# Optimization experiments

Hardware: AMD Instinct MI355X
Metric: run time of the kernel (lower is better)

Reference implementation:

```python
import jax, jax.numpy as jnp
import numpy as np

H = 16          # n_heads
WIN = 256       # window_size
NEG_INF = -1e30 # finite stand-in for -inf to stay fp16/bf16 safe


def setup_inputs() -> dict:
    key = jax.random.key(0)
    ks = jax.random.split(key, 9)
    B, L, C = 2, 2048, 2048
    s = 0.02  # weight init scale
    inp = {
        "x": jax.random.normal(ks[0], (B, L, C), jnp.float32),
        "Wq": jax.random.normal(ks[1], (C, C), jnp.float32) * s,
        "bq": jnp.zeros((C,), jnp.float32),
        "Wk": jax.random.normal(ks[2], (C, C), jnp.float32) * s,
        "bk": jnp.zeros((C,), jnp.float32),
        "Wv": jax.random.normal(ks[3], (C, C), jnp.float32) * s,
        "bv": jnp.zeros((C,), jnp.float32),
        "Wo": jax.random.normal(ks[4], (C, C), jnp.float32) * s,
        "bo": jnp.zeros((C,), jnp.float32),
    }
    return inp


def _attn(x, Wq, bq, Wk, bk, Wv, bv, Wo, bo):
    B, L, C = x.shape
    D = C // H
    # torch Linear: y = x @ W.T + b
    q = (x @ Wq.T + bq).reshape(B, L, H, D).transpose(0, 2, 1, 3)  # (B,H,L,D)
    k = (x @ Wk.T + bk).reshape(B, L, H, D).transpose(0, 2, 1, 3)
    v = (x @ Wv.T + bv).reshape(B, L, H, D).transpose(0, 2, 1, 3)
    i = jnp.arange(L)[:, None]
    j = jnp.arange(L)[None, :]
    allowed = (j <= i) & (j > i - WIN)
    bias = jnp.where(allowed, 0.0, NEG_INF).astype(x.dtype)  # (L,L)
    scale = 1.0 / np.sqrt(D)
    attn = jnp.einsum('bhid,bhjd->bhij', q, k) + bias
    a = jax.nn.softmax(attn * scale, axis=-1)
    out = jnp.einsum('bhij,bhjd->bhid', a, v)  # (B,H,L,D)
    out = out.transpose(0, 2, 1, 3).reshape(B, L, C)
    return out @ Wo.T + bo  # dropout = identity (eval mode)


def reference(x, Wq, bq, Wk, bk, Wv, bv, Wo, bo):
    return _attn(x, Wq, bq, Wk, bk, Wv, bv, Wo, bo)
```

## Files before the change

### kernel.cpp

```cpp
#include <hip/hip_runtime.h>
#include <hip/hip_bf16.h>
#include <stdint.h>

typedef __bf16 bf16;
typedef __attribute__((ext_vector_type(8))) __bf16 bf16x8;
typedef __attribute__((ext_vector_type(8))) unsigned short u16x8;
typedef __attribute__((ext_vector_type(4))) float f32x4;

#define L_SEQ 2048
#define C_DIM 2048
#define NBATCH 2
#define M_ROWS (NBATCH * L_SEQ)
#define DH 128
#define NHEAD 16
#define WINSZ 256

__device__ __forceinline__ float san(float v, float s) {
    return ((__float_as_uint(v) & 0x7f800000u) == 0x7f800000u) ? s : v;
}

__device__ __forceinline__ bf16x8 pack8(float4 lo, float4 hi) {
    bf16x8 v;
    v[0] = (bf16)lo.x; v[1] = (bf16)lo.y; v[2] = (bf16)lo.z; v[3] = (bf16)lo.w;
    v[4] = (bf16)hi.x; v[5] = (bf16)hi.y; v[6] = (bf16)hi.z; v[7] = (bf16)hi.w;
    return v;
}

typedef const __attribute__((address_space(1))) void g_void;
typedef __attribute__((address_space(3))) void l_void;
__device__ __forceinline__ void glds16(const void* g, void* l) {
    __builtin_amdgcn_global_load_lds((g_void*)g, (l_void*)l, 16, 0, 0);
}

template <bool AF32, bool OUTF32>
__global__ __launch_bounds__(256)
void gemm_bt_bias(const void* __restrict__ Ap,
                  const float* __restrict__ W0, const float* __restrict__ b0, void* O0,
                  const float* __restrict__ W1, const float* __restrict__ b1, void* O1,
                  const float* __restrict__ W2, const float* __restrict__ b2, void* O2,
                  float snt)
{
    const int K = C_DIM, N = C_DIM;
    const float* W = W0; const float* bias = b0; void* Out = O0;
    if (blockIdx.z == 1)      { W = W1; bias = b1; Out = O1; }
    else if (blockIdx.z == 2) { W = W2; bias = b2; Out = O2; }

    __shared__ bf16 As[128 * 32];
    __shared__ bf16 Bs[128 * 32];

    const int tid  = threadIdx.x;
    const int lane = tid & 63;
    const int m0 = blockIdx.x * 128;
    const int n0 = blockIdx.y * 128;

    const int wave = tid >> 6;
    const int wm = (wave >> 1) * 64;
    const int wn = (wave & 1) * 64;

    const int srow = tid >> 2;
    const int scol = (tid & 3) * 8;

    f32x4 acc[4][4] = {};

    const int fr = lane & 15;
    const int fq = (lane >> 4) * 8;

    for (int k0 = 0; k0 < K; k0 += 32) {
        bf16x8 ra[2], rb[2];
        #pragma unroll
        for (int p = 0; p < 2; p++) {
            const size_t aoff = (size_t)(m0 + p * 64 + srow) * K + k0 + scol;
            if (AF32) {
                const float* A = (const float*)Ap;
                float4 lo = *(const float4*)(A + aoff);
                float4 hi = *(const float4*)(A + aoff + 4);
                ra[p] = pack8(lo, hi);
            } else {
                const bf16* A = (const bf16*)Ap;
                ra[p] = *(const bf16x8*)(A + aoff);
            }
            const size_t boff = (size_t)(n0 + p * 64 + srow) * K + k0 + scol;
            float4 wlo = *(const float4*)(W + boff);
            float4 whi = *(const float4*)(W + boff + 4);
            rb[p] = pack8(wlo, whi);
        }
        __syncthreads();
        #pragma unroll
        for (int p = 0; p < 2; p++) {
            *(bf16x8*)&As[(p * 64 + srow) * 32 + scol] = ra[p];
            *(bf16x8*)&Bs[(p * 64 + srow) * 32 + scol] = rb[p];
        }
        __syncthreads();

        bf16x8 af[4], bfr[4];
        #pragma unroll
        for (int s = 0; s < 4; s++)
            af[s] = *(const bf16x8*)&As[(wm + s * 16 + fr) * 32 + fq];
        #pragma unroll
        for (int s = 0; s < 4; s++)
            bfr[s] = *(const bf16x8*)&Bs[(wn + s * 16 + fr) * 32 + fq];
        #pragma unroll
        for (int sm = 0; sm < 4; sm++)
            #pragma unroll
            for (int sn = 0; sn < 4; sn++)
                acc[sm][sn] = __builtin_amdgcn_mfma_f32_16x16x32_bf16(af[sm], bfr[sn], acc[sm][sn], 0, 0, 0);
    }

    const int r0 = (lane >> 4) * 4;
    const int cn = lane & 15;
    #pragma unroll
    for (int sn = 0; sn < 4; sn++) {
        const int n = n0 + wn + sn * 16 + cn;
        const float bv = bias[n];
        #pragma unroll
        for (int sm = 0; sm < 4; sm++) {
            const int m = m0 + wm + sm * 16 + r0;
            #pragma unroll
            for (int r = 0; r < 4; r++) {
                const float v = san(acc[sm][sn][r] + bv, snt);
                if (OUTF32) ((float*)Out)[(size_t)(m + r) * N + n] = v;
                else        ((bf16*)Out)[(size_t)(m + r) * N + n] = (bf16)v;
            }
        }
    }
}

__device__ __forceinline__ void phase_mid() {
    asm volatile("" ::: "memory");
    __builtin_amdgcn_s_barrier();
    asm volatile("s_waitcnt lgkmcnt(0)" ::: "memory");
    __builtin_amdgcn_sched_barrier(0);
    __builtin_amdgcn_s_setprio(1);
}
__device__ __forceinline__ void phase_end() {
    __builtin_amdgcn_s_setprio(0);
    asm volatile("" ::: "memory");
    __builtin_amdgcn_s_barrier();
}

#define BUFSZ 49152
#define BOFF  32768

#define LDA2(d) do {                                                          \
    char* s_ = lds + (d) * BUFSZ + ahalf * 16384;                             \
    _Pragma("unroll") for (int sm = 0; sm < 4; sm++)                          \
    _Pragma("unroll") for (int kk = 0; kk < 2; kk++) {                        \
        const int row_ = arow0 + sm * 16 + fr;                                \
        afr[sm][kk] = *(const bf16x8*)(s_ + row_ * 128 +                      \
                        (((kk * 4 + g) ^ (row_ & 7)) << 4));                  \
    } } while (0)

#define LDB2(d, qn, arr) do {                                                 \
    char* s_ = lds + (d) * BUFSZ + BOFF;                                      \
    _Pragma("unroll") for (int sn = 0; sn < 2; sn++)                          \
    _Pragma("unroll") for (int kk = 0; kk < 2; kk++) {                        \
        const int row_ = wn + (qn) * 32 + sn * 16 + fr;                       \
        arr[sn][kk] = *(const bf16x8*)(s_ + row_ * 128 +                      \
                        (((kk * 4 + g) ^ (row_ & 7)) << 4));                  \
    } } while (0)

#define MFMAH(qn, arr) do {                                                   \
    _Pragma("unroll") for (int kk = 0; kk < 2; kk++)                          \
    _Pragma("unroll") for (int sm = 0; sm < 4; sm++)                          \
    _Pragma("unroll") for (int sn = 0; sn < 2; sn++)                          \
        acc[sm][(qn) * 2 + sn] =                                              \
            __builtin_amdgcn_mfma_f32_16x16x32_bf16(afr[sm][kk], arr[sn][kk], \
                acc[sm][(qn) * 2 + sn], 0, 0, 0);                             \
    } while (0)

template <bool OUTF32>
__global__ __launch_bounds__(512, 2)
void gemm_256x128(const bf16* __restrict__ A,
                  const bf16* __restrict__ W0, const float* __restrict__ b0, void* O0,
                  const bf16* __restrict__ W1, const float* __restrict__ b1, void* O1,
                  const bf16* __restrict__ W2, const float* __restrict__ b2, void* O2,
                  float snt)
{
    const int K = C_DIM, N = C_DIM;
    const int NT = K / 64;
    const bf16* W = W0; const float* bias = b0; void* Out = O0;
    if (blockIdx.z == 1)      { W = W1; bias = b1; Out = O1; }
    else if (blockIdx.z == 2) { W = W2; bias = b2; Out = O2; }

    __shared__ __attribute__((aligned(16))) char lds[98304];

    const int tid  = threadIdx.x;
    const int lane = tid & 63;
    const int w    = tid >> 6;

    int id = blockIdx.x + (int)gridDim.x * blockIdx.y;
    id = (id & 7) * 32 + (id >> 3);
    const int m0 = (id & 15) * 256;
    const int n0 = (id >> 4) * 128;

    const int wm = (w >> 1) * 64;
    const int wn = (w & 1) * 64;
    const int fr = lane & 15;
    const int g  = lane >> 4;
    const int ahalf = w >> 2;
    const int arow0 = ((w >> 1) & 1) * 64;

    const int srow  = tid >> 3;
    const int scol  = (((tid & 7) ^ (srow & 7)) * 8);
    const int wvoff = (tid >> 6) * 1024;

    f32x4 acc[4][4] = {};
    bf16x8 afr[4][2], b0r[2][2], b1r[2][2];

    #define STAGE_A(t) do {                                                   \
        const int d_ = (t) & 1;                                               \
        const int tc_ = (t) < NT ? (t) : NT - 1;                              \
        const bf16* src_ = A + (size_t)(m0 + srow) * K + tc_ * 64 + scol;     \
        char* dst_ = lds + d_ * BUFSZ + wvoff;                                \
        glds16(src_,                   dst_);                                 \
        glds16(src_ + (size_t)64 * K,  dst_ + 8192);                          \
        glds16(src_ + (size_t)128 * K, dst_ + 16384);                         \
        glds16(src_ + (size_t)192 * K, dst_ + 24576);                         \
    } while (0)

    #define STAGE_B(t) do {                                                   \
        const int d_ = (t) & 1;                                               \
        const int tc_ = (t) < NT ? (t) : NT - 1;                              \
        const bf16* src_ = W + (size_t)(n0 + srow) * K + tc_ * 64 + scol;     \
        char* dst_ = lds + d_ * BUFSZ + BOFF + wvoff;                         \
        glds16(src_,                  dst_);                                  \
        glds16(src_ + (size_t)64 * K, dst_ + 8192);                           \
    } while (0)

    STAGE_A(0); STAGE_B(0); STAGE_A(1);
    asm volatile("s_waitcnt vmcnt(4)" ::: "memory");
    asm volatile("" ::: "memory");
    __builtin_amdgcn_s_barrier();

    #pragma unroll 1
    for (int i = 0; i < NT / 2; i++) {
        const int t1 = 2 * i + 1, t2 = 2 * i + 2, t3 = 2 * i + 3;
        LDA2(0); LDB2(0, 0, b0r);
        STAGE_B(t1);
        phase_mid(); MFMAH(0, b0r); phase_end();
        LDB2(0, 1, b1r);
        STAGE_A(t2);
        asm volatile("s_waitcnt vmcnt(4)" ::: "memory");
        phase_mid(); MFMAH(1, b1r); phase_end();
        LDA2(1); LDB2(1, 0, b0r);
        STAGE_B(t2);
        phase_mid(); MFMAH(0, b0r); phase_end();
        LDB2(1, 1, b1r);
        STAGE_A(t3);
        asm volatile("s_waitcnt vmcnt(4)" ::: "memory");
        phase_mid(); MFMAH(1, b1r); phase_end();
    }
    asm volatile("s_waitcnt vmcnt(0)" ::: "memory");

    const int cn = lane & 15;
    const int r0 = (lane >> 4) * 4;
    #pragma unroll
    for (int sn2 = 0; sn2 < 4; sn2++) {
        const int n = n0 + wn + sn2 * 16 + cn;
        const float bv = bias[n];
        #pragma unroll
        for (int sm2 = 0; sm2 < 4; sm2++) {
            const int m = m0 + wm + sm2 * 16 + r0;
            #pragma unroll
            for (int r = 0; r < 4; r++) {
                const float v = san(acc[sm2][sn2][r] + bv, snt);
                if (OUTF32) ((float*)Out)[(size_t)(m + r) * N + n] = v;
                else        ((bf16*)Out)[(size_t)(m + r) * N + n] = (bf16)v;
            }
        }
    }
    #undef STAGE_A
    #undef STAGE_B
}

__global__ __launch_bounds__(256)
void cvt_f32_bf16(const float* __restrict__ s0, bf16* __restrict__ d0,
                  const float* __restrict__ s1, bf16* __restrict__ d1,
                  const float* __restrict__ s2, bf16* __restrict__ d2,
                  const float* __restrict__ s3, bf16* __restrict__ d3,
                  const float* __restrict__ s4, bf16* __restrict__ d4)
{
    const float* s; bf16* d; int n;
    switch (blockIdx.y) {
        case 0:  s = s0; d = d0; n = M_ROWS * C_DIM; break;
        case 1:  s = s1; d = d1; n = C_DIM * C_DIM; break;
        case 2:  s = s2; d = d2; n = C_DIM * C_DIM; break;
        case 3:  s = s3; d = d3; n = C_DIM * C_DIM; break;
        default: s = s4; d = d4; n = C_DIM * C_DIM; break;
    }
    const int nv = n >> 3;
    const int stride = (int)gridDim.x * 256;
    for (int i = blockIdx.x * 256 + threadIdx.x; i < nv; i += stride) {
        const float4 lo = *(const float4*)(s + (size_t)i * 8);
        const float4 hi = *(const float4*)(s + (size_t)i * 8 + 4);
        *(bf16x8*)(d + (size_t)i * 8) = pack8(lo, hi);
    }
}

#define SWZK(r, byteoff) ((((r) * 256) + (byteoff)) ^ (((r) & 7) << 4))
#define SWZV(d, byteoff) ((((d) * 128) + (byteoff)) ^ (((((d) & 7) ^ (((d) >> 3) & 7))) << 4))
#define SWZP(r, byteoff) ((((r) * 128) + (byteoff)) ^ (((r) & 7) << 4))

__global__ __launch_bounds__(256)
void swa_attn(const bf16* __restrict__ Q, const bf16* __restrict__ Kp,
              const bf16* __restrict__ V, bf16* __restrict__ Oattn, float snt)
{
    __shared__ bf16 Ks[64 * 128];
    __shared__ bf16 Vt[128 * 64];
    __shared__ bf16 Ps[64 * 64];

    const int tid  = threadIdx.x;
    const int lane = tid & 63;
    const int w    = tid >> 6;
    const int q0 = blockIdx.x * 64;
    const int h  = blockIdx.y;
    const int b  = blockIdx.z;
    const size_t base = (size_t)b * L_SEQ * C_DIM + (size_t)h * DH;

    const int fr  = lane & 15;
    const int g   = lane >> 4;
    const int fq8 = g * 8;

    bf16x8 qf[4];
    {
        const bf16* qrow = Q + base + (size_t)(q0 + w * 16 + fr) * C_DIM;
        #pragma unroll
        for (int kk = 0; kk < 4; kk++)
            qf[kk] = *(const bf16x8*)(qrow + kk * 32 + fq8);
    }

    const int rl0 = g * 4;
    const int ig  = q0 + w * 16 + rl0;
    const float scale = 0.08838834764831845f;

    float m_run[4], l_run[4];
    #pragma unroll
    for (int r = 0; r < 4; r++) { m_run[r] = -1e30f; l_run[r] = 0.0f; }
    f32x4 Oacc[8] = {};

    const int krr = tid >> 4;
    const int kcc = (tid & 15) * 8;
    const int vc  = tid & 15;
    const int vd0 = vc * 8;
    const int vpb = tid >> 4;

    for (int kb = 0; kb < 5; kb++) {
        const int s = q0 - 256 + kb * 64;
        if (s < 0) continue;

        __syncthreads();

        #pragma unroll
        for (int p = 0; p < 4; p++) {
            const int r = p * 16 + krr;
            const uint4 kv = *(const uint4*)(Kp + base + (size_t)(s + r) * C_DIM + kcc);
            *(uint4*)((char*)Ks + SWZK(r, kcc * 2)) = kv;
        }
        #pragma unroll
        for (int it = 0; it < 2; it++) {
            const int p = vpb + it * 16;
            const bf16* vr = V + base + (size_t)(s + 2 * p) * C_DIM + vd0;
            const u16x8 va = *(const u16x8*)vr;
            const u16x8 vb = *(const u16x8*)(vr + C_DIM);
            #pragma unroll
            for (int j = 0; j < 8; j++) {
                const uint32_t val = (uint32_t)va[j] | ((uint32_t)vb[j] << 16);
                *(uint32_t*)((char*)Vt + SWZV(vd0 + j, 4 * p)) = val;
            }
        }
        __syncthreads();

        f32x4 sacc[4] = {};
        __builtin_amdgcn_s_setprio(1);
        #pragma unroll
        for (int kk = 0; kk < 4; kk++) {
            #pragma unroll
            for (int t = 0; t < 4; t++) {
                const bf16x8 kf = *(const bf16x8*)((char*)Ks + SWZK(t * 16 + fr, (kk * 32 + fq8) * 2));
                sacc[t] = __builtin_amdgcn_mfma_f32_16x16x32_bf16(qf[kk], kf, sacc[t], 0, 0, 0);
            }
        }
        __builtin_amdgcn_s_setprio(0);

        float alpha[4];
        #pragma unroll
        for (int r = 0; r < 4; r++) {
            const int iq = ig + r;
            float p4[4];
            float bm = -1e30f;
            #pragma unroll
            for (int t = 0; t < 4; t++) {
                const int j = s + t * 16 + fr;
                const bool allow = (j <= iq) && (j > iq - WINSZ);
                p4[t] = allow ? sacc[t][r] * scale : -1e30f;
                bm = fmaxf(bm, p4[t]);
            }
            bm = fmaxf(bm, __shfl_xor(bm, 1, 64));
            bm = fmaxf(bm, __shfl_xor(bm, 2, 64));
            bm = fmaxf(bm, __shfl_xor(bm, 4, 64));
            bm = fmaxf(bm, __shfl_xor(bm, 8, 64));
            const float m_new = fmaxf(m_run[r], bm);
            alpha[r] = __expf(m_run[r] - m_new);
            m_run[r] = m_new;
            float ps = 0.0f;
            #pragma unroll
            for (int t = 0; t < 4; t++) {
                const float e = (p4[t] > -1e29f) ? __expf(p4[t] - m_new) : 0.0f;
                p4[t] = e;
                ps += e;
            }
            ps += __shfl_xor(ps, 1, 64);
            ps += __shfl_xor(ps, 2, 64);
            ps += __shfl_xor(ps, 4, 64);
            ps += __shfl_xor(ps, 8, 64);
            l_run[r] = l_run[r] * alpha[r] + ps;

            const int prow = w * 16 + rl0 + r;
            #pragma unroll
            for (int t = 0; t < 4; t++)
                *(bf16*)((char*)Ps + SWZP(prow, (t * 16 + fr) * 2)) = (bf16)p4[t];
        }

        #pragma unroll
        for (int t = 0; t < 8; t++)
            #pragma unroll
            for (int r = 0; r < 4; r++)
                Oacc[t][r] *= alpha[r];

        __builtin_amdgcn_s_setprio(1);
        #pragma unroll
        for (int kk = 0; kk < 2; kk++) {
            const bf16x8 pa = *(const bf16x8*)((char*)Ps + SWZP(w * 16 + fr, (kk * 32 + fq8) * 2));
            #pragma unroll
            for (int t = 0; t < 8; t++) {
                const bf16x8 vf = *(const bf16x8*)((char*)Vt + SWZV(t * 16 + fr, (kk * 32 + fq8) * 2));
                Oacc[t] = __builtin_amdgcn_mfma_f32_16x16x32_bf16(pa, vf, Oacc[t], 0, 0, 0);
            }
        }
        __builtin_amdgcn_s_setprio(0);
    }

    bf16* ob = Oattn + base;
    #pragma unroll
    for (int r = 0; r < 4; r++) {
        const float inv_l = 1.0f / l_run[r];
        const size_t ro = (size_t)(q0 + w * 16 + rl0 + r) * C_DIM;
        #pragma unroll
        for (int t = 0; t < 8; t++)
            ob[ro + t * 16 + fr] = (bf16)san(Oacc[t][r] * inv_l, snt);
    }
}

__global__ void fill_signal(float* out, int n, float v) {
    for (int i = blockIdx.x * blockDim.x + threadIdx.x; i < n; i += gridDim.x * blockDim.x)
        out[i] = v;
}

extern "C" void kernel_launch(void* const* d_in, const int* in_sizes, int n_in,
                              void* d_out, int out_size, void* d_ws, size_t ws_size,
                              hipStream_t stream) {
    const size_t sz      = (size_t)M_ROWS * C_DIM;
    const size_t wsz     = (size_t)C_DIM * C_DIM;
    const size_t bfbytes = sz * sizeof(bf16);
    const size_t FASTNEED = 3 * sz * sizeof(bf16) + 4 * wsz * sizeof(bf16);

    const int expn[9] = {8388608, 4194304, 2048, 4194304, 2048,
                         4194304, 2048, 4194304, 2048};
    float sig = 0.0f;
    if (n_in != 9) sig = 1100.0f;
    else {
        for (int i = 0; i < 9; i++)
            if (in_sizes[i] != expn[i]) { sig = 1200.0f + 100.0f * i; break; }
    }
    if (sig == 0.0f && out_size != (int)sz) sig = 2100.0f;
    if (sig == 0.0f && ws_size < 2 * bfbytes) sig = 3000.0f + 10.0f * (float)(ws_size >> 20);
    if (sig != 0.0f) {
        fill_signal<<<512, 256, 0, stream>>>((float*)d_out, (int)sz, sig);
        return;
    }

    const float* x  = (const float*)d_in[0];
    const float* Wq = (const float*)d_in[1];
    const float* bq = (const float*)d_in[2];
    const float* Wk = (const float*)d_in[3];
    const float* bk = (const float*)d_in[4];
    const float* Wv = (const float*)d_in[5];
    const float* bv = (const float*)d_in[6];
    const float* Wo = (const float*)d_in[7];
    const float* bo = (const float*)d_in[8];

    if (ws_size >= FASTNEED) {
        bf16* xbf = (bf16*)d_ws;
        bf16* kws = xbf + sz;
        bf16* vws = kws + sz;
        bf16* wqb = vws + sz;
        bf16* wkb = wqb + wsz;
        bf16* wvb = wkb + wsz;
        bf16* wob = wvb + wsz;
        bf16*  qscr  = (bf16*)d_out;
        float* out32 = (float*)d_out;

        cvt_f32_bf16<<<dim3(2048, 5), 256, 0, stream>>>(
            x, xbf, Wq, wqb, Wk, wkb, Wv, wvb, Wo, wob);

        gemm_256x128<false><<<dim3(16, 16, 3), 512, 0, stream>>>(
            xbf, wqb, bq, (void*)qscr, wkb, bk, (void*)kws,
            wvb, bv, (void*)vws, 111.0f);

        swa_attn<<<dim3(L_SEQ / 64, NHEAD, NBATCH), 256, 0, stream>>>(
            qscr, kws, vws, xbf, 222.0f);

        gemm_256x128<true><<<dim3(16, 16, 1), 512, 0, stream>>>(
            xbf, wob, bo, (void*)out32, wob, bo, (void*)out32,
            wob, bo, (void*)out32, 444.0f);
    } else {
        bf16*  kws   = (bf16*)d_ws;
        bf16*  vws   = kws + sz;
        bf16*  qscr  = (bf16*)d_out;
        float* out32 = (float*)d_out;

        gemm_bt_bias<true, false><<<dim3(32, 16, 3), 256, 0, stream>>>(
            (const void*)x, Wq, bq, (void*)qscr, Wk, bk, (void*)kws,
            Wv, bv, (void*)vws, 111.0f);

        swa_attn<<<dim3(L_SEQ / 64, NHEAD, NBATCH), 256, 0, stream>>>(
            qscr, kws, vws, qscr, 222.0f);

        hipMemcpyAsync(kws, qscr, bfbytes, hipMemcpyDeviceToDevice, stream);

        gemm_bt_bias<false, true><<<dim3(32, 16, 1), 256, 0, stream>>>(
            (const void*)kws, Wo, bo, (void*)out32, Wo, bo, (void*)out32,
            Wo, bo, (void*)out32, 444.0f);
    }
}
```

Measured before the change: 329.5 us.

## Load K tiles via global_load_lds and prefetch next V block into registers

In the sliding-window attention kernel, K tiles are now copied straight from global memory into LDS with global_load_lds. A pre-swizzled column index replaces the load-to-register-then-store path. V rows for the next key block are loaded into registers while the current block is computed, which overlaps global latency with the QK/PV MFMA work. The loop now starts at the first valid key block instead of testing and skipping negative starts. The cost is extra live registers for the prefetched V, and correctness depends on the direct-to-LDS write layout matching the SWZK swizzle the reads expect.

```diff
diff --git a/kernel.cpp b/kernel.cpp
--- a/kernel.cpp
+++ b/kernel.cpp
@@ -30,6 +30,19 @@
 typedef __attribute__((address_space(3))) void l_void;
 __device__ __forceinline__ void glds16(const void* g, void* l) {
     __builtin_amdgcn_global_load_lds((g_void*)g, (l_void*)l, 16, 0, 0);
+}
+
+__device__ __forceinline__ void phase_mid() {
+    asm volatile("" ::: "memory");
+    __builtin_amdgcn_s_barrier();
+    asm volatile("s_waitcnt lgkmcnt(0)" ::: "memory");
+    __builtin_amdgcn_sched_barrier(0);
+    __builtin_amdgcn_s_setprio(1);
+}
+__device__ __forceinline__ void phase_end() {
+    __builtin_amdgcn_s_setprio(0);
+    asm volatile("" ::: "memory");
+    __builtin_amdgcn_s_barrier();
 }
 
 template <bool AF32, bool OUTF32>
@@ -123,19 +136,6 @@
             }
         }
     }
-}
-
-__device__ __forceinline__ void phase_mid() {
-    asm volatile("" ::: "memory");
-    __builtin_amdgcn_s_barrier();
-    asm volatile("s_waitcnt lgkmcnt(0)" ::: "memory");
-    __builtin_amdgcn_sched_barrier(0);
-    __builtin_amdgcn_s_setprio(1);
-}
-__device__ __forceinline__ void phase_end() {
-    __builtin_amdgcn_s_setprio(0);
-    asm volatile("" ::: "memory");
-    __builtin_amdgcn_s_barrier();
 }
 
 #define BUFSZ 49152
@@ -338,37 +338,54 @@
     for (int r = 0; r < 4; r++) { m_run[r] = -1e30f; l_run[r] = 0.0f; }
     f32x4 Oacc[8] = {};
 
-    const int krr = tid >> 4;
-    const int kcc = (tid & 15) * 8;
-    const int vc  = tid & 15;
-    const int vd0 = vc * 8;
+    const int krow = tid >> 4;
+    const int kcol = ((tid & 15) ^ (krow & 7)) * 8;
+    char* const kdst = (char*)Ks + w * 1024;
+
+    const int vd0 = (tid & 15) * 8;
     const int vpb = tid >> 4;
 
-    for (int kb = 0; kb < 5; kb++) {
+    const int kbs = (blockIdx.x < 4) ? (4 - (int)blockIdx.x) : 0;
+
+    u16x8 va0, vb0, va1, vb1;
+    {
+        const int s0 = q0 - 256 + kbs * 64;
+        const bf16* vr0 = V + base + (size_t)(s0 + 2 * vpb) * C_DIM + vd0;
+        va0 = *(const u16x8*)vr0;
+        vb0 = *(const u16x8*)(vr0 + C_DIM);
+        const bf16* vr1 = V + base + (size_t)(s0 + 2 * (vpb + 16)) * C_DIM + vd0;
+        va1 = *(const u16x8*)vr1;
+        vb1 = *(const u16x8*)(vr1 + C_DIM);
+    }
+
+    for (int kb = kbs; kb < 5; kb++) {
         const int s = q0 - 256 + kb * 64;
-        if (s < 0) continue;
 
         __syncthreads();
 
         #pragma unroll
-        for (int p = 0; p < 4; p++) {
-            const int r = p * 16 + krr;
-            const uint4 kv = *(const uint4*)(Kp + base + (size_t)(s + r) * C_DIM + kcc);
-            *(uint4*)((char*)Ks + SWZK(r, kcc * 2)) = kv;
-        }
-        #pragma unroll
-        for (int it = 0; it < 2; it++) {
-            const int p = vpb + it * 16;
-            const bf16* vr = V + base + (size_t)(s + 2 * p) * C_DIM + vd0;
-            const u16x8 va = *(const u16x8*)vr;
-            const u16x8 vb = *(const u16x8*)(vr + C_DIM);
-            #pragma unroll
-            for (int j = 0; j < 8; j++) {
-                const uint32_t val = (uint32_t)va[j] | ((uint32_t)vb[j] << 16);
-                *(uint32_t*)((char*)Vt + SWZV(vd0 + j, 4 * p)) = val;
-            }
+        for (int p = 0; p < 4; p++)
+            glds16(Kp + base + (size_t)(s + p * 16 + krow) * C_DIM + kcol,
+                   kdst + p * 4096);
+
+        #pragma unroll
+        for (int j = 0; j < 8; j++) {
+            const uint32_t v0 = (uint32_t)va0[j] | ((uint32_t)vb0[j] << 16);
+            *(uint32_t*)((char*)Vt + SWZV(vd0 + j, 4 * vpb)) = v0;
+            const uint32_t v1 = (uint32_t)va1[j] | ((uint32_t)vb1[j] << 16);
+            *(uint32_t*)((char*)Vt + SWZV(vd0 + j, 4 * (vpb + 16))) = v1;
         }
         __syncthreads();
+
+        if (kb < 4) {
+            const int sn = s + 64;
+            const bf16* vr0 = V + base + (size_t)(sn + 2 * vpb) * C_DIM + vd0;
+            va0 = *(const u16x8*)vr0;
+            vb0 = *(const u16x8*)(vr0 + C_DIM);
+            const bf16* vr1 = V + base + (size_t)(sn + 2 * (vpb + 16)) * C_DIM + vd0;
+            va1 = *(const u16x8*)vr1;
+            vb1 = *(const u16x8*)(vr1 + C_DIM);
+        }
 
         f32x4 sacc[4] = {};
         __builtin_amdgcn_s_setprio(1);
```

Result: slower. 356.7 us (+8.2%).

## Enlarge attention query tile to 128 rows with 8 waves and skip inactive waves

Applied to the files above, without the earlier changes.

The sliding-window attention kernel now handles 128 query rows per block with 512 threads (8 waves), so each K/V tile loaded into shared memory serves twice as many queries. Each block now walks 6 key tiles instead of 5. Waves whose 16 query rows fall outside a key tile's window skip the QK, softmax and PV work. The block index is also remapped so that neighbouring blocks are spread across XCDs. The cost is a larger P buffer in shared memory and fewer, larger blocks (512 in total). The attention kernel is only part of the total time, which also includes the GEMMs.

```diff
diff --git a/kernel.cpp b/kernel.cpp
--- a/kernel.cpp
+++ b/kernel.cpp
@@ -30,6 +30,19 @@
 typedef __attribute__((address_space(3))) void l_void;
 __device__ __forceinline__ void glds16(const void* g, void* l) {
     __builtin_amdgcn_global_load_lds((g_void*)g, (l_void*)l, 16, 0, 0);
+}
+
+__device__ __forceinline__ void phase_mid() {
+    asm volatile("" ::: "memory");
+    __builtin_amdgcn_s_barrier();
+    asm volatile("s_waitcnt lgkmcnt(0)" ::: "memory");
+    __builtin_amdgcn_sched_barrier(0);
+    __builtin_amdgcn_s_setprio(1);
+}
+__device__ __forceinline__ void phase_end() {
+    __builtin_amdgcn_s_setprio(0);
+    asm volatile("" ::: "memory");
+    __builtin_amdgcn_s_barrier();
 }
 
 template <bool AF32, bool OUTF32>
@@ -123,19 +136,6 @@
             }
         }
     }
-}
-
-__device__ __forceinline__ void phase_mid() {
-    asm volatile("" ::: "memory");
-    __builtin_amdgcn_s_barrier();
-    asm volatile("s_waitcnt lgkmcnt(0)" ::: "memory");
-    __builtin_amdgcn_sched_barrier(0);
-    __builtin_amdgcn_s_setprio(1);
-}
-__device__ __forceinline__ void phase_end() {
-    __builtin_amdgcn_s_setprio(0);
-    asm volatile("" ::: "memory");
-    __builtin_amdgcn_s_barrier();
 }
 
 #define BUFSZ 49152
@@ -301,36 +301,43 @@
 #define SWZV(d, byteoff) ((((d) * 128) + (byteoff)) ^ (((((d) & 7) ^ (((d) >> 3) & 7))) << 4))
 #define SWZP(r, byteoff) ((((r) * 128) + (byteoff)) ^ (((r) & 7) << 4))
 
-__global__ __launch_bounds__(256)
+__global__ __launch_bounds__(512)
 void swa_attn(const bf16* __restrict__ Q, const bf16* __restrict__ Kp,
               const bf16* __restrict__ V, bf16* __restrict__ Oattn, float snt)
 {
     __shared__ bf16 Ks[64 * 128];
     __shared__ bf16 Vt[128 * 64];
-    __shared__ bf16 Ps[64 * 64];
+    __shared__ bf16 Ps[128 * 64];
 
     const int tid  = threadIdx.x;
     const int lane = tid & 63;
     const int w    = tid >> 6;
-    const int q0 = blockIdx.x * 64;
-    const int h  = blockIdx.y;
-    const int b  = blockIdx.z;
+
+    int f = blockIdx.x + 16 * (blockIdx.y + 16 * blockIdx.z);
+    f = (f & 7) * 64 + (f >> 3);
+    const int bx = f & 15;
+    const int h  = (f >> 4) & 15;
+    const int b  = f >> 8;
+
+    const int q0 = bx * 128;
     const size_t base = (size_t)b * L_SEQ * C_DIM + (size_t)h * DH;
 
     const int fr  = lane & 15;
     const int g   = lane >> 4;
     const int fq8 = g * 8;
 
+    const int qw = q0 + w * 16;
+
     bf16x8 qf[4];
     {
-        const bf16* qrow = Q + base + (size_t)(q0 + w * 16 + fr) * C_DIM;
+        const bf16* qrow = Q + base + (size_t)(qw + fr) * C_DIM;
         #pragma unroll
         for (int kk = 0; kk < 4; kk++)
             qf[kk] = *(const bf16x8*)(qrow + kk * 32 + fq8);
     }
 
     const int rl0 = g * 4;
-    const int ig  = q0 + w * 16 + rl0;
+    const int ig  = qw + rl0;
     const float scale = 0.08838834764831845f;
 
     float m_run[4], l_run[4];
@@ -340,111 +347,111 @@
 
     const int krr = tid >> 4;
     const int kcc = (tid & 15) * 8;
-    const int vc  = tid & 15;
-    const int vd0 = vc * 8;
+    const int vd0 = (tid & 15) * 8;
     const int vpb = tid >> 4;
 
-    for (int kb = 0; kb < 5; kb++) {
+    for (int kb = 0; kb < 6; kb++) {
         const int s = q0 - 256 + kb * 64;
         if (s < 0) continue;
 
         __syncthreads();
 
         #pragma unroll
-        for (int p = 0; p < 4; p++) {
-            const int r = p * 16 + krr;
+        for (int p = 0; p < 2; p++) {
+            const int r = p * 32 + krr;
             const uint4 kv = *(const uint4*)(Kp + base + (size_t)(s + r) * C_DIM + kcc);
             *(uint4*)((char*)Ks + SWZK(r, kcc * 2)) = kv;
         }
-        #pragma unroll
-        for (int it = 0; it < 2; it++) {
-            const int p = vpb + it * 16;
-            const bf16* vr = V + base + (size_t)(s + 2 * p) * C_DIM + vd0;
+        {
+            const bf16* vr = V + base + (size_t)(s + 2 * vpb) * C_DIM + vd0;
             const u16x8 va = *(const u16x8*)vr;
             const u16x8 vb = *(const u16x8*)(vr + C_DIM);
             #pragma unroll
             for (int j = 0; j < 8; j++) {
                 const uint32_t val = (uint32_t)va[j] | ((uint32_t)vb[j] << 16);
-                *(uint32_t*)((char*)Vt + SWZV(vd0 + j, 4 * p)) = val;
+                *(uint32_t*)((char*)Vt + SWZV(vd0 + j, 4 * vpb)) = val;
             }
         }
         __syncthreads();
 
-        f32x4 sacc[4] = {};
-        __builtin_amdgcn_s_setprio(1);
-        #pragma unroll
-        for (int kk = 0; kk < 4; kk++) {
-            #pragma unroll
-            for (int t = 0; t < 4; t++) {
-                const bf16x8 kf = *(const bf16x8*)((char*)Ks + SWZK(t * 16 + fr, (kk * 32 + fq8) * 2));
-                sacc[t] = __builtin_amdgcn_mfma_f32_16x16x32_bf16(qf[kk], kf, sacc[t], 0, 0, 0);
-            }
-        }
-        __builtin_amdgcn_s_setprio(0);
-
-        float alpha[4];
-        #pragma unroll
-        for (int r = 0; r < 4; r++) {
-            const int iq = ig + r;
-            float p4[4];
-            float bm = -1e30f;
-            #pragma unroll
-            for (int t = 0; t < 4; t++) {
-                const int j = s + t * 16 + fr;
-                const bool allow = (j <= iq) && (j > iq - WINSZ);
-                p4[t] = allow ? sacc[t][r] * scale : -1e30f;
-                bm = fmaxf(bm, p4[t]);
-            }
-            bm = fmaxf(bm, __shfl_xor(bm, 1, 64));
-            bm = fmaxf(bm, __shfl_xor(bm, 2, 64));
-            bm = fmaxf(bm, __shfl_xor(bm, 4, 64));
-            bm = fmaxf(bm, __shfl_xor(bm, 8, 64));
-            const float m_new = fmaxf(m_run[r], bm);
-            alpha[r] = __expf(m_run[r] - m_new);
-            m_run[r] = m_new;
-            float ps = 0.0f;
-            #pragma unroll
-            for (int t = 0; t < 4; t++) {
-                const float e = (p4[t] > -1e29f) ? __expf(p4[t] - m_new) : 0.0f;
-                p4[t] = e;
-                ps += e;
-            }
-            ps += __shfl_xor(ps, 1, 64);
-            ps += __shfl_xor(ps, 2, 64);
-            ps += __shfl_xor(ps, 4, 64);
-            ps += __shfl_xor(ps, 8, 64);
-            l_run[r] = l_run[r] * alpha[r] + ps;
-
-            const int prow = w * 16 + rl0 + r;
-            #pragma unroll
-            for (int t = 0; t < 4; t++)
-                *(bf16*)((char*)Ps + SWZP(prow, (t * 16 + fr) * 2)) = (bf16)p4[t];
-        }
-
-        #pragma unroll
-        for (int t = 0; t < 8; t++)
-            #pragma unroll
-            for (int r = 0; r < 4; r++)
-                Oacc[t][r] *= alpha[r];
-
-        __builtin_amdgcn_s_setprio(1);
-        #pragma unroll
-        for (int kk = 0; kk < 2; kk++) {
-            const bf16x8 pa = *(const bf16x8*)((char*)Ps + SWZP(w * 16 + fr, (kk * 32 + fq8) * 2));
-            #pragma unroll
-            for (int t = 0; t < 8; t++) {
-                const bf16x8 vf = *(const bf16x8*)((char*)Vt + SWZV(t * 16 + fr, (kk * 32 + fq8) * 2));
-                Oacc[t] = __builtin_amdgcn_mfma_f32_16x16x32_bf16(pa, vf, Oacc[t], 0, 0, 0);
-            }
-        }
-        __builtin_amdgcn_s_setprio(0);
+        const bool wactive = (s <= qw + 15) && (s + 63 > qw - 256);
+        if (wactive) {
+            f32x4 sacc[4] = {};
+            __builtin_amdgcn_s_setprio(1);
+            #pragma unroll
+            for (int kk = 0; kk < 4; kk++) {
+                #pragma unroll
+                for (int t = 0; t < 4; t++) {
+                    const bf16x8 kf = *(const bf16x8*)((char*)Ks + SWZK(t * 16 + fr, (kk * 32 + fq8) * 2));
+                    sacc[t] = __builtin_amdgcn_mfma_f32_16x16x32_bf16(qf[kk], kf, sacc[t], 0, 0, 0);
+                }
+            }
+            __builtin_amdgcn_s_setprio(0);
+
+            float alpha[4];
+            #pragma unroll
+            for (int r = 0; r < 4; r++) {
+                const int iq = ig + r;
+                float p4[4];
+                float bm = -1e30f;
+                #pragma unroll
+                for (int t = 0; t < 4; t++) {
+                    const int j = s + t * 16 + fr;
+                    const bool allow = (j <= iq) && (j > iq - WINSZ);
+                    p4[t] = allow ? sacc[t][r] * scale : -1e30f;
+                    bm = fmaxf(bm, p4[t]);
+                }
+                bm = fmaxf(bm, __shfl_xor(bm, 1, 64));
+                bm = fmaxf(bm, __shfl_xor(bm, 2, 64));
+                bm = fmaxf(bm, __shfl_xor(bm, 4, 64));
+                bm = fmaxf(bm, __shfl_xor(bm, 8, 64));
+                const float m_new = fmaxf(m_run[r], bm);
+                alpha[r] = __expf(m_run[r] - m_new);
+                m_run[r] = m_new;
+                float ps = 0.0f;
+                #pragma unroll
+                for (int t = 0; t < 4; t++) {
+                    const float e = (p4[t] > -1e29f) ? __expf(p4[t] - m_new) : 0.0f;
+                    p4[t] = e;
+                    ps += e;
+                }
+                ps += __shfl_xor(ps, 1, 64);
+                ps += __shfl_xor(ps, 2, 64);
+                ps += __shfl_xor(ps, 4, 64);
+                ps += __shfl_xor(ps, 8, 64);
+                l_run[r] = l_run[r] * alpha[r] + ps;
+
+                const int prow = w * 16 + rl0 + r;
+                #pragma unroll
+                for (int t = 0; t < 4; t++)
+                    *(bf16*)((char*)Ps + SWZP(prow, (t * 16 + fr) * 2)) = (bf16)p4[t];
+            }
+
+            #pragma unroll
+            for (int t = 0; t < 8; t++)
+                #pragma unroll
+                for (int r = 0; r < 4; r++)
+                    Oacc[t][r] *= alpha[r];
+
+            __builtin_amdgcn_s_setprio(1);
+            #pragma unroll
+            for (int kk = 0; kk < 2; kk++) {
+                const bf16x8 pa = *(const bf16x8*)((char*)Ps + SWZP(w * 16 + fr, (kk * 32 + fq8) * 2));
+                #pragma unroll
+                for (int t = 0; t < 8; t++) {
+                    const bf16x8 vf = *(const bf16x8*)((char*)Vt + SWZV(t * 16 + fr, (kk * 32 + fq8) * 2));
+                    Oacc[t] = __builtin_amdgcn_mfma_f32_16x16x32_bf16(pa, vf, Oacc[t], 0, 0, 0);
+                }
+            }
+            __builtin_amdgcn_s_setprio(0);
+        }
     }
 
     bf16* ob = Oattn + base;
     #pragma unroll
     for (int r = 0; r < 4; r++) {
         const float inv_l = 1.0f / l_run[r];
-        const size_t ro = (size_t)(q0 + w * 16 + rl0 + r) * C_DIM;
+        const size_t ro = (size_t)(qw + rl0 + r) * C_DIM;
         #pragma unroll
         for (int t = 0; t < 8; t++)
             ob[ro + t * 16 + fr] = (bf16)san(Oacc[t][r] * inv_l, snt);
@@ -507,7 +514,7 @@
             xbf, wqb, bq, (void*)qscr, wkb, bk, (void*)kws,
             wvb, bv, (void*)vws, 111.0f);
 
-        swa_attn<<<dim3(L_SEQ / 64, NHEAD, NBATCH), 256, 0, stream>>>(
+        swa_attn<<<dim3(L_SEQ / 128, NHEAD, NBATCH), 512, 0, stream>>>(
             qscr, kws, vws, xbf, 222.0f);
 
         gemm_256x128<true><<<dim3(16, 16, 1), 512, 0, stream>>>(
@@ -523,7 +530,7 @@
             (const void*)x, Wq, bq, (void*)qscr, Wk, bk, (void*)kws,
             Wv, bv, (void*)vws, 111.0f);
 
-        swa_attn<<<dim3(L_SEQ / 64, NHEAD, NBATCH), 256, 0, stream>>>(
+        swa_attn<<<dim3(L_SEQ / 128, NHEAD, NBATCH), 512, 0, stream>>>(
             qscr, kws, vws, qscr, 222.0f);
 
         hipMemcpyAsync(kws, qscr, bfbytes, hipMemcpyDeviceToDevice, stream);
```

New measurement: 340.3 us. +3.3%, slower.
